# Kernel optimization log

Measured on AMD Instinct MI355X. Metric: run time of the kernel, lower is better.

The kernel has to match this reference:

```python
import jax, jax.numpy as jnp
import numpy as np

# --- constants matching vis_net(scale=1) ---
SCALE = 1.0
L = 8                      # n_levels
F = 2                      # n_features_per_level
LOG2_T = 19
T = 1 << LOG2_T            # hash table size per level
N_MIN = 32                 # base_resolution
B = float(np.exp(np.log(2048.0 * SCALE / N_MIN) / (L - 1)))  # per_level_scale

PRIMES = jnp.array([1, 2654435761, 805459861], dtype=jnp.uint32)
# 8 corners of the unit cube
OFFSETS = jnp.array([[(c >> d) & 1 for d in range(3)] for c in range(8)], dtype=jnp.uint32)  # [8,3]


def _hash(coords):
    # coords: [N,8,3] uint32 -> [N,8] int32 indices into table of size T
    h = coords * PRIMES                      # uint32 wraps, as in tcnn
    h = h[..., 0] ^ h[..., 1] ^ h[..., 2]
    return (h & jnp.uint32(T - 1)).astype(jnp.int32)


def _encode(x01, table):
    # x01: [N,3] in [0,1]; table: [L,T,F]
    feats = []
    for l in range(L):
        scale_l = N_MIN * (B ** l) - 1.0     # tcnn grid scale for level l
        pos = x01 * scale_l + 0.5            # [N,3]
        p0 = jnp.floor(pos)
        w = pos - p0                         # trilinear fractions [N,3]
        corners = p0.astype(jnp.uint32)[:, None, :] + OFFSETS[None, :, :]  # [N,8,3]
        idx = _hash(corners)                 # [N,8]
        f = table[l][idx]                    # gather -> [N,8,F]
        wt = jnp.prod(jnp.where(OFFSETS[None].astype(bool), w[:, None, :], 1.0 - w[:, None, :]), axis=-1)  # [N,8]
        feats.append(jnp.sum(f * wt[..., None], axis=1))  # [N,F]
    return jnp.concatenate(feats, axis=-1)   # [N, L*F] = [N,16]


def setup_inputs() -> dict:
    key = jax.random.key(0)
    k0, k1, k2, k3 = jax.random.split(key, 4)
    N = 4_194_304
    x = jax.random.uniform(k0, (N, 3), jnp.float32, -SCALE, SCALE)
    # tcnn initializes hash features uniform in [-1e-4, 1e-4]
    table = jax.random.uniform(k1, (L, T, F), jnp.float32, -1e-4, 1e-4)
    W1 = jax.random.normal(k2, (L * F, 32), jnp.float32) * (1.0 / np.sqrt(L * F))
    b1 = jnp.zeros((32,), jnp.float32)
    W2 = jax.random.normal(k3, (32, 1), jnp.float32) * (1.0 / np.sqrt(32))
    b2 = jnp.zeros((1,), jnp.float32)
    return {"x": x, "table": table, "W1": W1, "b1": b1, "W2": W2, "b2": b2}


def reference(x, table, W1, b1, W2, b2):
    # normalize to [0,1] as in forward: (x - xyz_min) / (xyz_max - xyz_min)
    x01 = (x + SCALE) / (2.0 * SCALE)
    enc = _encode(x01, table)                      # [N,16]
    h = jax.nn.relu(enc @ W1 + b1)                 # [N,32]
    vis = jax.nn.sigmoid(h @ W2 + b2)              # [N,1]
    return vis[:, 0]
```

## Files before the change

kernel.cpp:

```cpp
#include <hip/hip_runtime.h>
#include <hip/hip_bf16.h>
#include <math.h>

#define NLVL 8
#define LOG2T 19
#define TSZ (1u << LOG2T)

struct Scales { float s[NLVL]; };

static __device__ __forceinline__ unsigned short f2bf(float f) {
    unsigned u = __builtin_bit_cast(unsigned, f);
    u += 0x7fffu + ((u >> 16) & 1u);
    return (unsigned short)(u >> 16);
}
static __device__ __forceinline__ float bfbits2f(unsigned hi16) {
    return __builtin_bit_cast(float, hi16);
}

__global__ __launch_bounds__(256) void encode_kernel(
    const float* __restrict__ x,
    const float* __restrict__ table,
    unsigned* __restrict__ encb,
    int N, Scales sc)
{
    const int lvl = blockIdx.x & 7;
    const int i = (blockIdx.x >> 3) * blockDim.x + threadIdx.x;
    if (i >= N) return;

    float xx = __builtin_nontemporal_load(x + 3 * i + 0);
    float yy = __builtin_nontemporal_load(x + 3 * i + 1);
    float zz = __builtin_nontemporal_load(x + 3 * i + 2);
    float px = (xx + 1.0f) * 0.5f;
    float py = (yy + 1.0f) * 0.5f;
    float pz = (zz + 1.0f) * 0.5f;

    const float s = sc.s[lvl];
    float fx = fmaf(px, s, 0.5f);
    float fy = fmaf(py, s, 0.5f);
    float fz = fmaf(pz, s, 0.5f);
    float bx = floorf(fx), by = floorf(fy), bz = floorf(fz);
    float wx = fx - bx, wy = fy - by, wz = fz - bz;
    unsigned cx = (unsigned)bx, cy = (unsigned)by, cz = (unsigned)bz;

    unsigned hy0 = cy * 2654435761u;
    unsigned hy1 = hy0 + 2654435761u;
    unsigned hz0 = cz * 805459861u;
    unsigned hz1 = hz0 + 805459861u;
    unsigned cx1 = cx + 1u;
    const unsigned m = TSZ - 1u;
    const float2* tl = reinterpret_cast<const float2*>(table) + (size_t)lvl * TSZ;

    float2 f000 = tl[(cx  ^ hy0 ^ hz0) & m];
    float2 f100 = tl[(cx1 ^ hy0 ^ hz0) & m];
    float2 f010 = tl[(cx  ^ hy1 ^ hz0) & m];
    float2 f110 = tl[(cx1 ^ hy1 ^ hz0) & m];
    float2 f001 = tl[(cx  ^ hy0 ^ hz1) & m];
    float2 f101 = tl[(cx1 ^ hy0 ^ hz1) & m];
    float2 f011 = tl[(cx  ^ hy1 ^ hz1) & m];
    float2 f111 = tl[(cx1 ^ hy1 ^ hz1) & m];

    float wx0 = 1.0f - wx, wy0 = 1.0f - wy, wz0 = 1.0f - wz;
    float w00 = wx0 * wy0, w10 = wx * wy0, w01 = wx0 * wy, w11 = wx * wy;
    float a000 = w00 * wz0, a100 = w10 * wz0, a010 = w01 * wz0, a110 = w11 * wz0;
    float a001 = w00 * wz,  a101 = w10 * wz,  a011 = w01 * wz,  a111 = w11 * wz;

    float e0 = fmaf(f000.x, a000,
               fmaf(f100.x, a100,
               fmaf(f010.x, a010,
               fmaf(f110.x, a110,
               fmaf(f001.x, a001,
               fmaf(f101.x, a101,
               fmaf(f011.x, a011, f111.x * a111)))))));
    float e1 = fmaf(f000.y, a000,
               fmaf(f100.y, a100,
               fmaf(f010.y, a010,
               fmaf(f110.y, a110,
               fmaf(f001.y, a001,
               fmaf(f101.y, a101,
               fmaf(f011.y, a011, f111.y * a111)))))));

    unsigned pk = ((unsigned)f2bf(e1) << 16) | (unsigned)f2bf(e0);
    __builtin_nontemporal_store(pk, encb + (size_t)lvl * N + i);
}

__global__ __launch_bounds__(256) void mlp_kernel(
    const unsigned* __restrict__ encb,
    const float* __restrict__ W1,
    const float* __restrict__ b1,
    const float* __restrict__ W2,
    const float* __restrict__ b2,
    float* __restrict__ out, int N)
{
    int i = blockIdx.x * blockDim.x + threadIdx.x;
    if (i >= N) return;

    float enc[16];
    #pragma unroll
    for (int l = 0; l < NLVL; ++l) {
        unsigned pk = __builtin_nontemporal_load(encb + (size_t)l * N + i);
        enc[2 * l + 0] = bfbits2f(pk << 16);
        enc[2 * l + 1] = bfbits2f(pk & 0xffff0000u);
    }

    float h[32];
    #pragma unroll
    for (int j = 0; j < 32; ++j) h[j] = b1[j];
    #pragma unroll
    for (int k = 0; k < 16; ++k) {
        float e = enc[k];
        #pragma unroll
        for (int j = 0; j < 32; ++j)
            h[j] = fmaf(e, W1[k * 32 + j], h[j]);
    }
    float z = b2[0];
    #pragma unroll
    for (int j = 0; j < 32; ++j)
        z = fmaf(fmaxf(h[j], 0.0f), W2[j], z);

    out[i] = 1.0f / (1.0f + __expf(-z));
}

__global__ __launch_bounds__(256) void fused_kernel(
    const float* __restrict__ x, const float* __restrict__ table,
    const float* __restrict__ W1, const float* __restrict__ b1,
    const float* __restrict__ W2, const float* __restrict__ b2,
    float* __restrict__ out, int N, Scales sc)
{
    int i = blockIdx.x * blockDim.x + threadIdx.x;
    if (i >= N) return;
    float px = (x[3 * i + 0] + 1.0f) * 0.5f;
    float py = (x[3 * i + 1] + 1.0f) * 0.5f;
    float pz = (x[3 * i + 2] + 1.0f) * 0.5f;
    float enc[16];
    #pragma unroll
    for (int l = 0; l < NLVL; ++l) {
        const float s = sc.s[l];
        float fx = fmaf(px, s, 0.5f), fy = fmaf(py, s, 0.5f), fz = fmaf(pz, s, 0.5f);
        float bx = floorf(fx), by = floorf(fy), bz = floorf(fz);
        float wx = fx - bx, wy = fy - by, wz = fz - bz;
        unsigned cx = (unsigned)bx, cy = (unsigned)by, cz = (unsigned)bz;
        unsigned hy0 = cy * 2654435761u, hy1 = hy0 + 2654435761u;
        unsigned hz0 = cz * 805459861u, hz1 = hz0 + 805459861u;
        unsigned cx1 = cx + 1u;
        const unsigned m = TSZ - 1u;
        const float2* tl = reinterpret_cast<const float2*>(table) + (size_t)l * TSZ;
        float2 f000 = tl[(cx ^ hy0 ^ hz0) & m], f100 = tl[(cx1 ^ hy0 ^ hz0) & m];
        float2 f010 = tl[(cx ^ hy1 ^ hz0) & m], f110 = tl[(cx1 ^ hy1 ^ hz0) & m];
        float2 f001 = tl[(cx ^ hy0 ^ hz1) & m], f101 = tl[(cx1 ^ hy0 ^ hz1) & m];
        float2 f011 = tl[(cx ^ hy1 ^ hz1) & m], f111 = tl[(cx1 ^ hy1 ^ hz1) & m];
        float wx0 = 1.0f - wx, wy0 = 1.0f - wy, wz0 = 1.0f - wz;
        float w00 = wx0 * wy0, w10 = wx * wy0, w01 = wx0 * wy, w11 = wx * wy;
        float a000 = w00 * wz0, a100 = w10 * wz0, a010 = w01 * wz0, a110 = w11 * wz0;
        float a001 = w00 * wz, a101 = w10 * wz, a011 = w01 * wz, a111 = w11 * wz;
        enc[2*l+0] = fmaf(f000.x,a000, fmaf(f100.x,a100, fmaf(f010.x,a010, fmaf(f110.x,a110,
                     fmaf(f001.x,a001, fmaf(f101.x,a101, fmaf(f011.x,a011, f111.x*a111)))))));
        enc[2*l+1] = fmaf(f000.y,a000, fmaf(f100.y,a100, fmaf(f010.y,a010, fmaf(f110.y,a110,
                     fmaf(f001.y,a001, fmaf(f101.y,a101, fmaf(f011.y,a011, f111.y*a111)))))));
    }
    float h[32];
    #pragma unroll
    for (int j = 0; j < 32; ++j) h[j] = b1[j];
    #pragma unroll
    for (int k = 0; k < 16; ++k) {
        float e = enc[k];
        #pragma unroll
        for (int j = 0; j < 32; ++j) h[j] = fmaf(e, W1[k * 32 + j], h[j]);
    }
    float z = b2[0];
    #pragma unroll
    for (int j = 0; j < 32; ++j) z = fmaf(fmaxf(h[j], 0.0f), W2[j], z);
    out[i] = 1.0f / (1.0f + __expf(-z));
}

extern "C" void kernel_launch(void* const* d_in, const int* in_sizes, int n_in,
                              void* d_out, int out_size, void* d_ws, size_t ws_size,
                              hipStream_t stream) {
    const float* x     = (const float*)d_in[0];
    const float* table = (const float*)d_in[1];
    const float* W1    = (const float*)d_in[2];
    const float* b1    = (const float*)d_in[3];
    const float* W2    = (const float*)d_in[4];
    const float* b2    = (const float*)d_in[5];
    float* out = (float*)d_out;

    int N = in_sizes[0] / 3;

    Scales sc;
    double B = exp(log(2048.0 / 32.0) / 7.0);
    for (int l = 0; l < NLVL; ++l)
        sc.s[l] = (float)(32.0 * pow(B, (double)l) - 1.0);

    const int block = 256;
    const int chunks = (N + block - 1) / block;
    size_t need = (size_t)NLVL * (size_t)N * sizeof(unsigned);

    if (ws_size >= need) {
        unsigned* encb = (unsigned*)d_ws;
        encode_kernel<<<chunks * NLVL, block, 0, stream>>>(x, table, encb, N, sc);
        mlp_kernel<<<chunks, block, 0, stream>>>(encb, W1, b1, W2, b2, out, N);
    } else {
        fused_kernel<<<chunks, block, 0, stream>>>(x, table, W1, b1, W2, b2, out, N, sc);
    }
}
```

Baseline: 830.8 us.

## Convert hash table to packed fp16 before encoding to halve gather footprint

Adds a per-call conversion kernel that packs each level's two fp32 features into one 32-bit fp16 pair in workspace. The encode kernel then gathers 4-byte entries instead of 8-byte ones, halving the per-level table from 4 MB to 2 MB so it fits better in cache and cuts random-gather traffic. The cost is an extra pass reading 32 MB and writing 16 MB each call, plus fp16 rounding of the table values. The original fp32 path stays as a fallback when workspace is too small.

Measured after the change: 1.045 ms. 25.8% more time.

```diff
diff --git a/kernel.cpp b/kernel.cpp
--- a/kernel.cpp
+++ b/kernel.cpp
@@ -5,6 +5,9 @@
 #define NLVL 8
 #define LOG2T 19
 #define TSZ (1u << LOG2T)
+
+typedef float    f32x2 __attribute__((ext_vector_type(2)));
+typedef _Float16 f16x2 __attribute__((ext_vector_type(2)));
 
 struct Scales { float s[NLVL]; };
 
@@ -17,9 +20,24 @@
     return __builtin_bit_cast(float, hi16);
 }
 
-__global__ __launch_bounds__(256) void encode_kernel(
+__global__ __launch_bounds__(256) void cvt_kernel(
+    const float* __restrict__ table,
+    unsigned* __restrict__ tableh,
+    int LT)
+{
+    int e = blockIdx.x * blockDim.x + threadIdx.x;
+    if (e >= LT) return;
+    f32x2 v = __builtin_nontemporal_load(reinterpret_cast<const f32x2*>(table) + e);
+    _Float16 h0 = (_Float16)v.x;
+    _Float16 h1 = (_Float16)v.y;
+    unsigned u = (unsigned)__builtin_bit_cast(unsigned short, h0)
+               | ((unsigned)__builtin_bit_cast(unsigned short, h1) << 16);
+    __builtin_nontemporal_store(u, tableh + e);
+}
+
+__global__ __launch_bounds__(256) void encode_kernel_h(
     const float* __restrict__ x,
-    const float* __restrict__ table,
+    const unsigned* __restrict__ tableh,
     unsigned* __restrict__ encb,
     int N, Scales sc)
 {
@@ -48,35 +66,102 @@
     unsigned hz1 = hz0 + 805459861u;
     unsigned cx1 = cx + 1u;
     const unsigned m = TSZ - 1u;
-    const float2* tl = reinterpret_cast<const float2*>(table) + (size_t)lvl * TSZ;
-
-    float2 f000 = tl[(cx  ^ hy0 ^ hz0) & m];
-    float2 f100 = tl[(cx1 ^ hy0 ^ hz0) & m];
-    float2 f010 = tl[(cx  ^ hy1 ^ hz0) & m];
-    float2 f110 = tl[(cx1 ^ hy1 ^ hz0) & m];
-    float2 f001 = tl[(cx  ^ hy0 ^ hz1) & m];
-    float2 f101 = tl[(cx1 ^ hy0 ^ hz1) & m];
-    float2 f011 = tl[(cx  ^ hy1 ^ hz1) & m];
-    float2 f111 = tl[(cx1 ^ hy1 ^ hz1) & m];
+    const unsigned* tl = tableh + (size_t)lvl * TSZ;
+
+    unsigned g000 = tl[(cx  ^ hy0 ^ hz0) & m];
+    unsigned g100 = tl[(cx1 ^ hy0 ^ hz0) & m];
+    unsigned g010 = tl[(cx  ^ hy1 ^ hz0) & m];
+    unsigned g110 = tl[(cx1 ^ hy1 ^ hz0) & m];
+    unsigned g001 = tl[(cx  ^ hy0 ^ hz1) & m];
+    unsigned g101 = tl[(cx1 ^ hy0 ^ hz1) & m];
+    unsigned g011 = tl[(cx  ^ hy1 ^ hz1) & m];
+    unsigned g111 = tl[(cx1 ^ hy1 ^ hz1) & m];
 
     float wx0 = 1.0f - wx, wy0 = 1.0f - wy, wz0 = 1.0f - wz;
     float w00 = wx0 * wy0, w10 = wx * wy0, w01 = wx0 * wy, w11 = wx * wy;
     float a000 = w00 * wz0, a100 = w10 * wz0, a010 = w01 * wz0, a110 = w11 * wz0;
     float a001 = w00 * wz,  a101 = w10 * wz,  a011 = w01 * wz,  a111 = w11 * wz;
 
-    float e0 = fmaf(f000.x, a000,
-               fmaf(f100.x, a100,
-               fmaf(f010.x, a010,
-               fmaf(f110.x, a110,
-               fmaf(f001.x, a001,
-               fmaf(f101.x, a101,
+    f16x2 h000 = __builtin_bit_cast(f16x2, g000);
+    f16x2 h100 = __builtin_bit_cast(f16x2, g100);
+    f16x2 h010 = __builtin_bit_cast(f16x2, g010);
+    f16x2 h110 = __builtin_bit_cast(f16x2, g110);
+    f16x2 h001 = __builtin_bit_cast(f16x2, g001);
+    f16x2 h101 = __builtin_bit_cast(f16x2, g101);
+    f16x2 h011 = __builtin_bit_cast(f16x2, g011);
+    f16x2 h111 = __builtin_bit_cast(f16x2, g111);
+
+    float e0 = fmaf((float)h000.x, a000,
+               fmaf((float)h100.x, a100,
+               fmaf((float)h010.x, a010,
+               fmaf((float)h110.x, a110,
+               fmaf((float)h001.x, a001,
+               fmaf((float)h101.x, a101,
+               fmaf((float)h011.x, a011, (float)h111.x * a111)))))));
+    float e1 = fmaf((float)h000.y, a000,
+               fmaf((float)h100.y, a100,
+               fmaf((float)h010.y, a010,
+               fmaf((float)h110.y, a110,
+               fmaf((float)h001.y, a001,
+               fmaf((float)h101.y, a101,
+               fmaf((float)h011.y, a011, (float)h111.y * a111)))))));
+
+    unsigned pk = ((unsigned)f2bf(e1) << 16) | (unsigned)f2bf(e0);
+    __builtin_nontemporal_store(pk, encb + (size_t)lvl * N + i);
+}
+
+__global__ __launch_bounds__(256) void encode_kernel(
+    const float* __restrict__ x,
+    const float* __restrict__ table,
+    unsigned* __restrict__ encb,
+    int N, Scales sc)
+{
+    const int lvl = blockIdx.x & 7;
+    const int i = (blockIdx.x >> 3) * blockDim.x + threadIdx.x;
+    if (i >= N) return;
+
+    float xx = __builtin_nontemporal_load(x + 3 * i + 0);
+    float yy = __builtin_nontemporal_load(x + 3 * i + 1);
+    float zz = __builtin_nontemporal_load(x + 3 * i + 2);
+    float px = (xx + 1.0f) * 0.5f;
+    float py = (yy + 1.0f) * 0.5f;
+    float pz = (zz + 1.0f) * 0.5f;
+
+    const float s = sc.s[lvl];
+    float fx = fmaf(px, s, 0.5f);
+    float fy = fmaf(py, s, 0.5f);
+    float fz = fmaf(pz, s, 0.5f);
+    float bx = floorf(fx), by = floorf(fy), bz = floorf(fz);
+    float wx = fx - bx, wy = fy - by, wz = fz - bz;
+    unsigned cx = (unsigned)bx, cy = (unsigned)by, cz = (unsigned)bz;
+
+    unsigned hy0 = cy * 2654435761u;
+    unsigned hy1 = hy0 + 2654435761u;
+    unsigned hz0 = cz * 805459861u;
+    unsigned hz1 = hz0 + 805459861u;
+    unsigned cx1 = cx + 1u;
+    const unsigned m = TSZ - 1u;
+    const f32x2* tl = reinterpret_cast<const f32x2*>(table) + (size_t)lvl * TSZ;
+
+    f32x2 f000 = tl[(cx  ^ hy0 ^ hz0) & m];
+    f32x2 f100 = tl[(cx1 ^ hy0 ^ hz0) & m];
+    f32x2 f010 = tl[(cx  ^ hy1 ^ hz0) & m];
+    f32x2 f110 = tl[(cx1 ^ hy1 ^ hz0) & m];
+    f32x2 f001 = tl[(cx  ^ hy0 ^ hz1) & m];
+    f32x2 f101 = tl[(cx1 ^ hy0 ^ hz1) & m];
+    f32x2 f011 = tl[(cx  ^ hy1 ^ hz1) & m];
+    f32x2 f111 = tl[(cx1 ^ hy1 ^ hz1) & m];
+
+    float wx0 = 1.0f - wx, wy0 = 1.0f - wy, wz0 = 1.0f - wz;
+    float w00 = wx0 * wy0, w10 = wx * wy0, w01 = wx0 * wy, w11 = wx * wy;
+    float a000 = w00 * wz0, a100 = w10 * wz0, a010 = w01 * wz0, a110 = w11 * wz0;
+    float a001 = w00 * wz,  a101 = w10 * wz,  a011 = w01 * wz,  a111 = w11 * wz;
+
+    float e0 = fmaf(f000.x, a000, fmaf(f100.x, a100, fmaf(f010.x, a010,
+               fmaf(f110.x, a110, fmaf(f001.x, a001, fmaf(f101.x, a101,
                fmaf(f011.x, a011, f111.x * a111)))))));
-    float e1 = fmaf(f000.y, a000,
-               fmaf(f100.y, a100,
-               fmaf(f010.y, a010,
-               fmaf(f110.y, a110,
-               fmaf(f001.y, a001,
-               fmaf(f101.y, a101,
+    float e1 = fmaf(f000.y, a000, fmaf(f100.y, a100, fmaf(f010.y, a010,
+               fmaf(f110.y, a110, fmaf(f001.y, a001, fmaf(f101.y, a101,
                fmaf(f011.y, a011, f111.y * a111)))))));
 
     unsigned pk = ((unsigned)f2bf(e1) << 16) | (unsigned)f2bf(e0);
@@ -143,11 +228,11 @@
         unsigned hz0 = cz * 805459861u, hz1 = hz0 + 805459861u;
         unsigned cx1 = cx + 1u;
         const unsigned m = TSZ - 1u;
-        const float2* tl = reinterpret_cast<const float2*>(table) + (size_t)l * TSZ;
-        float2 f000 = tl[(cx ^ hy0 ^ hz0) & m], f100 = tl[(cx1 ^ hy0 ^ hz0) & m];
-        float2 f010 = tl[(cx ^ hy1 ^ hz0) & m], f110 = tl[(cx1 ^ hy1 ^ hz0) & m];
-        float2 f001 = tl[(cx ^ hy0 ^ hz1) & m], f101 = tl[(cx1 ^ hy0 ^ hz1) & m];
-        float2 f011 = tl[(cx ^ hy1 ^ hz1) & m], f111 = tl[(cx1 ^ hy1 ^ hz1) & m];
+        const f32x2* tl = reinterpret_cast<const f32x2*>(table) + (size_t)l * TSZ;
+        f32x2 f000 = tl[(cx ^ hy0 ^ hz0) & m], f100 = tl[(cx1 ^ hy0 ^ hz0) & m];
+        f32x2 f010 = tl[(cx ^ hy1 ^ hz0) & m], f110 = tl[(cx1 ^ hy1 ^ hz0) & m];
+        f32x2 f001 = tl[(cx ^ hy0 ^ hz1) & m], f101 = tl[(cx1 ^ hy0 ^ hz1) & m];
+        f32x2 f011 = tl[(cx ^ hy1 ^ hz1) & m], f111 = tl[(cx1 ^ hy1 ^ hz1) & m];
         float wx0 = 1.0f - wx, wy0 = 1.0f - wy, wz0 = 1.0f - wz;
         float w00 = wx0 * wy0, w10 = wx * wy0, w01 = wx0 * wy, w11 = wx * wy;
         float a000 = w00 * wz0, a100 = w10 * wz0, a010 = w01 * wz0, a110 = w11 * wz0;
@@ -192,9 +277,18 @@
 
     const int block = 256;
     const int chunks = (N + block - 1) / block;
-    size_t need = (size_t)NLVL * (size_t)N * sizeof(unsigned);
-
-    if (ws_size >= need) {
+    const int LT = NLVL * (int)TSZ;
+    const size_t tblh_bytes = (size_t)LT * 4;
+    const size_t encb_bytes = (size_t)NLVL * N * 4;
+    const size_t need_h = tblh_bytes + encb_bytes;
+
+    if (ws_size >= need_h) {
+        unsigned* tableh = (unsigned*)d_ws;
+        unsigned* encb = (unsigned*)((char*)d_ws + tblh_bytes);
+        cvt_kernel<<<LT / block, block, 0, stream>>>(table, tableh, LT);
+        encode_kernel_h<<<chunks * NLVL, block, 0, stream>>>(x, tableh, encb, N, sc);
+        mlp_kernel<<<chunks, block, 0, stream>>>(encb, W1, b1, W2, b2, out, N);
+    } else if (ws_size >= encb_bytes) {
         unsigned* encb = (unsigned*)d_ws;
         encode_kernel<<<chunks * NLVL, block, 0, stream>>>(x, table, encb, N, sc);
         mlp_kernel<<<chunks, block, 0, stream>>>(encb, W1, b1, W2, b2, out, N);
```
